# Optimization experiments

Hardware: AMD Instinct MI355X
Metric: run time of the kernel (lower is better)

## Reference

```python
import jax, jax.numpy as jnp
import numpy as np

N_NODES = 50000


def gcn_conv(x, edge_index, edge_weight, W, b):
    """PyG GCNConv: x' = D^{-1/2}(A+I)D^{-1/2} (x W) + b, with edge weights."""
    n = x.shape[0]
    x = x @ W  # transform first (PyG order): [N, d_out]
    row, col = edge_index[0], edge_index[1]  # source -> target
    # add self loops with weight 1
    loop = jnp.arange(n)
    row = jnp.concatenate([row, loop])
    col = jnp.concatenate([col, loop])
    ew = jnp.concatenate([edge_weight, jnp.ones((n,), dtype=x.dtype)])
    # symmetric normalization based on (weighted) in-degree at targets
    deg = jax.ops.segment_sum(ew, col, num_segments=n)
    dis = jnp.where(deg > 0, jax.lax.rsqrt(deg), 0.0)
    norm = dis[row] * ew * dis[col]  # [E+N]
    # gather-scale-scatter aggregation
    msg = x[row] * norm[:, None]  # [E+N, d_out]
    out = jax.ops.segment_sum(msg, col, num_segments=n)
    return out + b


def setup_inputs() -> dict:
    key = jax.random.key(0)
    ks = jax.random.split(key, 9)
    E = 800000
    bert_output = jax.random.normal(ks[0], (N_NODES, 1024), dtype=jnp.float32)
    edge_index = jax.random.randint(ks[1], (2, E), 0, N_NODES, dtype=jnp.int64)
    edge_weight = jax.random.uniform(ks[2], (E,), dtype=jnp.float32)
    s1 = 1.0 / np.sqrt(1024)
    s2 = 1.0 / np.sqrt(512)
    s3 = 1.0 / np.sqrt(128)
    W1 = jax.random.uniform(ks[3], (1024, 512), jnp.float32, -s1, s1)
    b1 = jnp.zeros((512,), jnp.float32)
    W2 = jax.random.uniform(ks[4], (512, 128), jnp.float32, -s2, s2)
    b2 = jnp.zeros((128,), jnp.float32)
    Wfc = jax.random.uniform(ks[5], (128, 14), jnp.float32, -s3, s3)
    bfc = jax.random.uniform(ks[6], (14,), jnp.float32, -s3, s3)
    return {
        "bert_output": bert_output,
        "edge_index": edge_index,
        "edge_weight": edge_weight,
        "W1": W1, "b1": b1, "W2": W2, "b2": b2, "Wfc": Wfc, "bfc": bfc,
    }


def reference(bert_output, edge_index, edge_weight, W1, b1, W2, b2, Wfc, bfc):
    h = jax.nn.relu(gcn_conv(bert_output, edge_index, edge_weight, W1, b1))
    h = jax.nn.relu(gcn_conv(h, edge_index, edge_weight, W2, b2))
    logits = h @ Wfc + bfc
    return jax.nn.sigmoid(logits)
```

## Files before the change

### kernel.cpp

```cpp
#include <hip/hip_runtime.h>
#include <stdint.h>

__device__ __forceinline__ float bf2f(unsigned short h) {
  union { uint32_t u; float f; } v; v.u = ((uint32_t)h) << 16; return v.f;
}
__device__ __forceinline__ unsigned short f2bf(float f) {
  union { float f; uint32_t u; } v; v.f = f;
  uint32_t u = v.u;
  u += 0x7FFFu + ((u >> 16) & 1u);
  return (unsigned short)(u >> 16);
}
__device__ __forceinline__ uint32_t pack2bf(float a, float b) {
  return (uint32_t)f2bf(a) | ((uint32_t)f2bf(b) << 16);
}
__device__ __forceinline__ int ld_idx(const void* p, size_t i, int is64) {
  return is64 ? (int)((const long long*)p)[i] : ((const int*)p)[i];
}
__device__ __forceinline__ float ld_w(const void* p, size_t i, int f32) {
  return f32 ? ((const float*)p)[i] : bf2f(((const unsigned short*)p)[i]);
}

typedef __attribute__((ext_vector_type(8))) short short8;
typedef __attribute__((ext_vector_type(4))) float floatx4;

__device__ __forceinline__ void gl2lds16(const unsigned short* g, unsigned short* l) {
  __builtin_amdgcn_global_load_lds(
      (const __attribute__((address_space(1))) uint32_t*)(const void*)g,
      (__attribute__((address_space(3))) uint32_t*)(void*)l,
      16, 0, 0);
}

__global__ void bgcn_init_probe(float* __restrict__ deg, int* __restrict__ counts,
                                int* __restrict__ fill, int n,
                                const uint32_t* __restrict__ xw,
                                const uint32_t* __restrict__ iw,
                                int* __restrict__ flags) {
  int i = blockIdx.x * 256 + threadIdx.x;
  if (i < n) { deg[i] = 1.0f; counts[i] = 0; fill[i] = 0; }
  if (blockIdx.x == 0 && threadIdx.x < 64) {
    int lane = threadIdx.x;
    int hits = 0;
    #pragma unroll
    for (int j = 0; j < 4; ++j) {
      uint32_t b = (xw[lane * 4 + j] >> 8) & 0x7F;
      hits += (b >= 0x38 && b <= 0x41) ? 1 : 0;
    }
    #pragma unroll
    for (int off = 32; off; off >>= 1) hits += __shfl_xor(hits, off);
    unsigned long long nz = __ballot(iw[2 * lane + 1] != 0u);
    if (lane == 0) {
      flags[0] = (hits < 128) ? 1 : 0;
      flags[1] = (nz == 0ull) ? 1 : 0;
    }
  }
}

__global__ void bgcn_cvt8(const void* __restrict__ src, unsigned short* __restrict__ dst,
                          int n8, const int* __restrict__ flags) {
  int i = blockIdx.x * 256 + threadIdx.x;
  if (i >= n8) return;
  size_t o = (size_t)i * 8;
  uint4 d;
  if (flags[0]) {
    const float4* f = (const float4*)((const float*)src + o);
    float4 f0 = f[0], f1 = f[1];
    d = make_uint4(pack2bf(f0.x, f0.y), pack2bf(f0.z, f0.w),
                   pack2bf(f1.x, f1.y), pack2bf(f1.z, f1.w));
  } else {
    d = *(const uint4*)((const unsigned short*)src + o);
  }
  *(uint4*)(dst + o) = d;
}
__global__ __launch_bounds__(256) void bgcn_cvt_t(
    const void* __restrict__ src, unsigned short* __restrict__ dst,
    int K, int N, const int* __restrict__ flags) {
  __shared__ unsigned short tile[32][33];
  int k0 = blockIdx.x * 32, n0 = blockIdx.y * 32;
  int tx = threadIdx.x & 31, ty = threadIdx.x >> 5;
  bool f32 = flags[0];
  #pragma unroll
  for (int i = 0; i < 4; ++i) {
    size_t s = (size_t)(k0 + ty + i * 8) * N + n0 + tx;
    tile[ty + i * 8][tx] = f32 ? f2bf(((const float*)src)[s])
                               : ((const unsigned short*)src)[s];
  }
  __syncthreads();
  #pragma unroll
  for (int i = 0; i < 4; ++i)
    dst[(size_t)(n0 + ty + i * 8) * K + k0 + tx] = tile[tx][ty + i * 8];
}
__global__ void bgcn_cvt_small(const void* b1, const void* b2,
                               const void* wfc, const void* bfc,
                               unsigned short* db1, unsigned short* db2,
                               unsigned short* dwfc, unsigned short* dbfc,
                               const int* __restrict__ flags) {
  int i = blockIdx.x * 256 + threadIdx.x;
  bool f32 = flags[0];
  const void* s; unsigned short* d; int j;
  if (i < 512)            { s = b1;  d = db1;  j = i; }
  else if (i < 640)       { s = b2;  d = db2;  j = i - 512; }
  else if (i < 2432)      { s = wfc; d = dwfc; j = i - 640; }
  else if (i < 2446)      { s = bfc; d = dbfc; j = i - 2432; }
  else return;
  d[j] = f32 ? f2bf(((const float*)s)[j]) : ((const unsigned short*)s)[j];
}

__global__ void bgcn_deg_hist(const void* __restrict__ ei, const void* __restrict__ ew,
                              const int* __restrict__ flags,
                              float* __restrict__ deg, int* __restrict__ counts, int E) {
  int e = blockIdx.x * 256 + threadIdx.x;
  if (e >= E) return;
  int c = ld_idx(ei, (size_t)E + e, flags[1]);
  atomicAdd(&deg[c], ld_w(ew, e, flags[0]));
  atomicAdd(&counts[c], 1);
}
__global__ void bgcn_scan_block(const int* __restrict__ counts, int* __restrict__ rowptr,
                                int* __restrict__ blocksum,
                                const float* __restrict__ deg, float* __restrict__ dis,
                                int n) {
  __shared__ int buf[1024];
  int gid = blockIdx.x * 1024 + threadIdx.x;
  int v = (gid < n) ? counts[gid] : 0;
  buf[threadIdx.x] = v;
  __syncthreads();
  for (int off = 1; off < 1024; off <<= 1) {
    int x = (threadIdx.x >= off) ? buf[threadIdx.x - off] : 0;
    __syncthreads();
    buf[threadIdx.x] += x;
    __syncthreads();
  }
  if (gid < n) {
    rowptr[gid + 1] = buf[threadIdx.x];
    dis[gid] = rsqrtf(deg[gid]);
  }
  if (threadIdx.x == 1023) blocksum[blockIdx.x] = buf[1023];
}
__global__ void bgcn_scan_tops(int* __restrict__ blocksum, int nb) {
  __shared__ int buf[1024];
  int t = threadIdx.x;
  int v = (t < nb) ? blocksum[t] : 0;
  buf[t] = v;
  __syncthreads();
  for (int off = 1; off < 1024; off <<= 1) {
    int x = (t >= off) ? buf[t - off] : 0;
    __syncthreads();
    buf[t] += x;
    __syncthreads();
  }
  if (t < nb) blocksum[t] = buf[t] - v;
}
__global__ void bgcn_scan_add(int* __restrict__ rowptr, const int* __restrict__ blocksum, int n) {
  int gid = blockIdx.x * 1024 + threadIdx.x;
  if (gid < n) rowptr[gid + 1] += blocksum[blockIdx.x];
  if (gid == 0) rowptr[0] = 0;
}
__global__ void bgcn_scatter(const void* __restrict__ ei, const void* __restrict__ ew,
                             const int* __restrict__ flags,
                             const float* __restrict__ dis,
                             const int* __restrict__ rowptr, int* __restrict__ fill,
                             int2* __restrict__ epair, int E) {
  int e = blockIdx.x * 256 + threadIdx.x;
  if (e >= E) return;
  int is64 = flags[1];
  int r = ld_idx(ei, e, is64), c = ld_idx(ei, (size_t)E + e, is64);
  int pos = rowptr[c] + atomicAdd(&fill[c], 1);
  float nrm = dis[r] * ld_w(ew, e, flags[0]) * dis[c];
  epair[pos] = make_int2(r, __float_as_int(nrm));
}

__global__ __launch_bounds__(256) void bgcn_gemm_lds(
    const unsigned short* __restrict__ A,
    const unsigned short* __restrict__ Bt,
    unsigned short* __restrict__ C,
    int M, int N, int K, int nblk_bits) {
  __shared__ unsigned short Abuf[128 * 32];
  __shared__ unsigned short Bbuf[128 * 32];
  int t = threadIdx.x;
  int wave = t >> 6, lane = t & 63;
  int bx = blockIdx.x;
  int nblk = bx & ((1 << nblk_bits) - 1);
  int mblk = bx >> nblk_bits;
  int m0 = mblk * 128, n0 = nblk * 128;

  floatx4 acc[4][4];
  #pragma unroll
  for (int i = 0; i < 4; ++i)
    #pragma unroll
    for (int j = 0; j < 4; ++j)
      #pragma unroll
      for (int r = 0; r < 4; ++r) acc[i][j][r] = 0.0f;

  int rii  = lane >> 2;
  int koff = (lane & 3) * 8;
  int ar0 = m0 + wave * 32 + rii;      if (ar0 >= M) ar0 = M - 1;
  int ar1 = m0 + wave * 32 + 16 + rii; if (ar1 >= M) ar1 = M - 1;
  const unsigned short* Ag0 = A + (size_t)ar0 * K + koff;
  const unsigned short* Ag1 = A + (size_t)ar1 * K + koff;
  const unsigned short* Bg0 = Bt + (size_t)(n0 + wave * 32 + rii) * K + koff;
  const unsigned short* Bg1 = Bg0 + (size_t)16 * K;
  unsigned short* Al0 = Abuf + (wave * 32) * 32 + lane * 8;
  unsigned short* Al1 = Abuf + (wave * 32 + 16) * 32 + lane * 8;
  unsigned short* Bl0 = Bbuf + (wave * 32) * 32 + lane * 8;
  unsigned short* Bl1 = Bbuf + (wave * 32 + 16) * 32 + lane * 8;

  int fr = lane & 15;
  int fk = (lane >> 4) * 8;
  int mw = (wave & 1) * 64;
  int nw = (wave >> 1) * 64;

  for (int k0 = 0; k0 < K; k0 += 32) {
    gl2lds16(Ag0 + k0, Al0);
    gl2lds16(Ag1 + k0, Al1);
    gl2lds16(Bg0 + k0, Bl0);
    gl2lds16(Bg1 + k0, Bl1);
    __syncthreads();

    short8 afr[4], bfr[4];
    #pragma unroll
    for (int i = 0; i < 4; ++i)
      afr[i] = *(const short8*)(Abuf + (mw + i * 16 + fr) * 32 + fk);
    #pragma unroll
    for (int i = 0; i < 4; ++i)
      bfr[i] = *(const short8*)(Bbuf + (nw + i * 16 + fr) * 32 + fk);
    #pragma unroll
    for (int mt = 0; mt < 4; ++mt)
      #pragma unroll
      for (int nt = 0; nt < 4; ++nt)
        acc[mt][nt] = __builtin_amdgcn_mfma_f32_16x16x32_bf16(afr[mt], bfr[nt], acc[mt][nt], 0, 0, 0);
    __syncthreads();
  }

  int col_l = lane & 15;
  int row_b = (lane >> 4) * 4;
  #pragma unroll
  for (int mt = 0; mt < 4; ++mt)
    #pragma unroll
    for (int nt = 0; nt < 4; ++nt)
      #pragma unroll
      for (int r = 0; r < 4; ++r) {
        int m = m0 + mw + mt * 16 + row_b + r;
        if (m < M)
          C[(size_t)m * N + n0 + nw + nt * 16 + col_l] = f2bf(acc[mt][nt][r]);
      }
}

#define GST 40
__global__ __launch_bounds__(256, 2) void bgcn_gemm128(
    const void* __restrict__ Araw, int a_probe, const int* __restrict__ flags,
    const unsigned short* __restrict__ Bt,
    unsigned short* __restrict__ C,
    int M, int N, int K, int nblk_bits) {
  __shared__ unsigned short Abuf[128 * GST];
  __shared__ unsigned short Bbuf[128 * GST];
  const bool a_fp32 = a_probe && flags[0];
  int t = threadIdx.x;
  int wave = t >> 6, lane = t & 63;
  int bx = blockIdx.x;
  int nblk = bx & ((1 << nblk_bits) - 1);
  int mblk = bx >> nblk_bits;
  int m0 = mblk * 128, n0 = nblk * 128;

  floatx4 acc[4][4];
  #pragma unroll
  for (int i = 0; i < 4; ++i)
    #pragma unroll
    for (int j = 0; j < 4; ++j)
      #pragma unroll
      for (int r = 0; r < 4; ++r) acc[i][j][r] = 0.0f;

  int srow  = t >> 1;
  int skoff = (t & 1) * 16;
  int am = m0 + srow; if (am >= M) am = M - 1;
  const float*          Af = (const float*)Araw          + (size_t)am * K + skoff;
  const unsigned short* Ah = (const unsigned short*)Araw + (size_t)am * K + skoff;
  const unsigned short* Bp = Bt + (size_t)(n0 + srow) * K + skoff;
  unsigned short* AL = Abuf + srow * GST + skoff;
  unsigned short* BL = Bbuf + srow * GST + skoff;

  int fr = lane & 15;
  int fk = (lane >> 4) * 8;
  int mw = (wave & 1) * 64;
  int nw = (wave >> 1) * 64;

  for (int k0 = 0; k0 < K; k0 += 32) {
    uint4 a0, a1;
    if (a_fp32) {
      float4 f0 = *(const float4*)(Af + k0);
      float4 f1 = *(const float4*)(Af + k0 + 4);
      float4 f2 = *(const float4*)(Af + k0 + 8);
      float4 f3 = *(const float4*)(Af + k0 + 12);
      a0 = make_uint4(pack2bf(f0.x, f0.y), pack2bf(f0.z, f0.w),
                      pack2bf(f1.x, f1.y), pack2bf(f1.z, f1.w));
      a1 = make_uint4(pack2bf(f2.x, f2.y), pack2bf(f2.z, f2.w),
                      pack2bf(f3.x, f3.y), pack2bf(f3.z, f3.w));
    } else {
      a0 = *(const uint4*)(Ah + k0);
      a1 = *(const uint4*)(Ah + k0 + 8);
    }
    uint4 b0 = *(const uint4*)(Bp + k0);
    uint4 b1 = *(const uint4*)(Bp + k0 + 8);
    *(uint4*)AL       = a0;
    *(uint4*)(AL + 8) = a1;
    *(uint4*)BL       = b0;
    *(uint4*)(BL + 8) = b1;
    __syncthreads();

    short8 afr[4], bfr[4];
    #pragma unroll
    for (int i = 0; i < 4; ++i)
      afr[i] = *(const short8*)(Abuf + (mw + i * 16 + fr) * GST + fk);
    #pragma unroll
    for (int i = 0; i < 4; ++i)
      bfr[i] = *(const short8*)(Bbuf + (nw + i * 16 + fr) * GST + fk);
    #pragma unroll
    for (int mt = 0; mt < 4; ++mt)
      #pragma unroll
      for (int nt = 0; nt < 4; ++nt)
        acc[mt][nt] = __builtin_amdgcn_mfma_f32_16x16x32_bf16(afr[mt], bfr[nt], acc[mt][nt], 0, 0, 0);
    __syncthreads();
  }

  int col_l = lane & 15;
  int row_b = (lane >> 4) * 4;
  #pragma unroll
  for (int mt = 0; mt < 4; ++mt)
    #pragma unroll
    for (int nt = 0; nt < 4; ++nt)
      #pragma unroll
      for (int r = 0; r < 4; ++r) {
        int m = m0 + mw + mt * 16 + row_b + r;
        if (m < M)
          C[(size_t)m * N + n0 + nw + nt * 16 + col_l] = f2bf(acc[mt][nt][r]);
      }
}

__device__ __forceinline__ void accum4(float* acc, uint2 r, float w) {
  acc[0] += w * bf2f((unsigned short)(r.x & 0xffff));
  acc[1] += w * bf2f((unsigned short)(r.x >> 16));
  acc[2] += w * bf2f((unsigned short)(r.y & 0xffff));
  acc[3] += w * bf2f((unsigned short)(r.y >> 16));
}
__device__ __forceinline__ void accum2(float* acc, uint32_t r, float w) {
  acc[0] += w * bf2f((unsigned short)(r & 0xffff));
  acc[1] += w * bf2f((unsigned short)(r >> 16));
}

template <int F, int WPN>
__global__ __launch_bounds__(256) void bgcn_aggregate(
    const unsigned short* __restrict__ H,
    const int* __restrict__ rowptr,
    const int2* __restrict__ epair,
    const float* __restrict__ dis,
    const unsigned short* __restrict__ bias,
    unsigned short* __restrict__ Out,
    int n_nodes) {
  constexpr int FPW = F / WPN;
  constexpr int VPL = FPW / 64;
  constexpr int NPB = 4 / WPN;
  constexpr int DEPTH = 8;

  int t = threadIdx.x;
  int lane = t & 63;
  int wid = __builtin_amdgcn_readfirstlane(t >> 6);
  int c = blockIdx.x * NPB + wid / WPN;
  if (c >= n_nodes) return;
  c = __builtin_amdgcn_readfirstlane(c);
  int h = wid % WPN;

  int beg = __builtin_amdgcn_readfirstlane(rowptr[c]);
  int end = __builtin_amdgcn_readfirstlane(rowptr[c + 1]);
  float ds = dis[c];

  int fo = h * FPW + lane * VPL;
  const unsigned short* Hl = H + fo;

  uint2 rs;
  union { uint2 v; unsigned short u[4]; } bu;
  if constexpr (VPL == 4) {
    rs = *(const uint2*)(Hl + (size_t)c * F);
    bu.v = *(const uint2*)(bias + fo);
  } else {
    rs.x = *(const uint32_t*)(Hl + (size_t)c * F);
    bu.v.x = *(const uint32_t*)(bias + fo);
  }

  float acc[VPL];
  #pragma unroll
  for (int j = 0; j < VPL; ++j) acc[j] = 0.0f;

  for (int base = beg; base < end; base += 64) {
    int n = end - base;
    if (n > 64) n = 64;
    n = __builtin_amdgcn_readfirstlane(n);
    int2 mv = make_int2(0, 0);
    if (lane < n) mv = epair[base + lane];
    for (int q0 = 0; q0 < n; q0 += DEPTH) {
      uint2 r[DEPTH];
      float w[DEPTH];
      #pragma unroll
      for (int j = 0; j < DEPTH; ++j) {
        int q = q0 + j;
        int qs = (q < n) ? q : 0;
        int sq = __builtin_amdgcn_readlane(mv.x, qs);
        w[j] = __int_as_float(
            __builtin_amdgcn_readlane(mv.y, q));
        const unsigned short* src = Hl + (size_t)sq * F;
        if constexpr (VPL == 4) r[j] = *(const uint2*)src;
        else                    r[j].x = *(const uint32_t*)src;
      }
      #pragma unroll
      for (int j = 0; j < DEPTH; ++j) {
        if constexpr (VPL == 4) accum4(acc, r[j], w[j]);
        else                    accum2(acc, r[j].x, w[j]);
      }
    }
  }

  float wself = ds * ds;
  if constexpr (VPL == 4) accum4(acc, rs, wself);
  else                    accum2(acc, rs.x, wself);

  unsigned short ob[VPL];
  #pragma unroll
  for (int j = 0; j < VPL; ++j) {
    float v = acc[j] + bf2f(bu.u[j]);
    ob[j] = f2bf(fmaxf(v, 0.0f));
  }
  if constexpr (VPL == 4) {
    uint2 st;
    st.x = (uint32_t)ob[0] | ((uint32_t)ob[1] << 16);
    st.y = (uint32_t)ob[2] | ((uint32_t)ob[3] << 16);
    *(uint2*)(Out + (size_t)c * F + fo) = st;
  } else {
    *(uint32_t*)(Out + (size_t)c * F + fo) =
        (uint32_t)ob[0] | ((uint32_t)ob[1] << 16);
  }
}

__global__ __launch_bounds__(256) void bgcn_fc_sigmoid(
    const unsigned short* __restrict__ X,
    const unsigned short* __restrict__ W,
    const unsigned short* __restrict__ b,
    float* __restrict__ out,
    int n_nodes) {
  __shared__ float Ws[128 * 14];
  __shared__ float bs[14];
  for (int i = threadIdx.x; i < 128 * 14; i += 256) Ws[i] = bf2f(W[i]);
  if (threadIdx.x < 14) bs[threadIdx.x] = bf2f(b[threadIdx.x]);
  __syncthreads();
  int node = blockIdx.x * 256 + threadIdx.x;
  if (node >= n_nodes) return;
  float acc[14];
  #pragma unroll
  for (int c = 0; c < 14; ++c) acc[c] = bs[c];
  const unsigned short* xp = X + (size_t)node * 128;
  for (int k8 = 0; k8 < 16; ++k8) {
    uint4 r = *(const uint4*)(xp + k8 * 8);
    float xv[8];
    xv[0] = bf2f((unsigned short)(r.x & 0xffff)); xv[1] = bf2f((unsigned short)(r.x >> 16));
    xv[2] = bf2f((unsigned short)(r.y & 0xffff)); xv[3] = bf2f((unsigned short)(r.y >> 16));
    xv[4] = bf2f((unsigned short)(r.z & 0xffff)); xv[5] = bf2f((unsigned short)(r.z >> 16));
    xv[6] = bf2f((unsigned short)(r.w & 0xffff)); xv[7] = bf2f((unsigned short)(r.w >> 16));
    #pragma unroll
    for (int j = 0; j < 8; ++j) {
      int k = k8 * 8 + j;
      #pragma unroll
      for (int c = 0; c < 14; ++c) acc[c] = fmaf(xv[j], Ws[k * 14 + c], acc[c]);
    }
  }
  float* op = out + (size_t)node * 14;
  #pragma unroll
  for (int c = 0; c < 14; ++c)
    op[c] = 1.0f / (1.0f + __expf(-acc[c]));
}

static inline size_t padsz(size_t x) { return (x + 255) & ~(size_t)255; }
static inline void* wsa(char*& p, size_t bytes) {
  void* r = p;
  p += padsz(bytes);
  return r;
}

extern "C" void kernel_launch(void* const* d_in, const int* in_sizes, int n_in,
                              void* d_out, int out_size, void* d_ws, size_t ws_size,
                              hipStream_t stream) {
  const void* Xr   = d_in[0];
  const void* EIr  = d_in[1];
  const void* EWr  = d_in[2];
  const void* W1r  = d_in[3];
  const void* b1r  = d_in[4];
  const void* W2r  = d_in[5];
  const void* b2r  = d_in[6];
  const void* Wfcr = d_in[7];
  const void* bfcr = d_in[8];
  float* out = (float*)d_out;

  const int N = in_sizes[0] / 1024;
  const int E = in_sizes[2];

  size_t need = padsz((size_t)N * 512 * 2)
              + padsz((size_t)N * 1024 * 2)
              + 4 * padsz((size_t)N * 4)
              + padsz((size_t)(N + 1) * 4)
              + padsz(256 * 4)
              + padsz((size_t)E * 8)
              + padsz(1024 * 512 * 2) + padsz(512 * 128 * 2)
              + padsz(512 * 2) + padsz(128 * 2) + padsz(128 * 14 * 2)
              + padsz(32) + padsz(8);
  const bool big = ws_size >= need;

  char* p = (char*)d_ws;
  unsigned short* R1  = (unsigned short*)wsa(p, (size_t)N * 512 * 2);
  unsigned short* R2  = (unsigned short*)wsa(p, (size_t)N * (big ? 1024 : 512) * 2);
  float* deg      = (float*)wsa(p, (size_t)N * 4);
  float* dis      = (float*)wsa(p, (size_t)N * 4);
  int*   counts   = (int*)wsa(p, (size_t)N * 4);
  int*   fill     = (int*)wsa(p, (size_t)N * 4);
  int*   rowptr   = (int*)wsa(p, (size_t)(N + 1) * 4);
  int*   blocksum = (int*)wsa(p, 256 * 4);
  int2*  epair    = (int2*)wsa(p, (size_t)E * 8);
  unsigned short* W1t  = (unsigned short*)wsa(p, (size_t)1024 * 512 * 2);
  unsigned short* W2t  = (unsigned short*)wsa(p, (size_t)512 * 128 * 2);
  unsigned short* b1c  = (unsigned short*)wsa(p, 512 * 2);
  unsigned short* b2c  = (unsigned short*)wsa(p, 128 * 2);
  unsigned short* Wfcc = (unsigned short*)wsa(p, 128 * 14 * 2);
  unsigned short* bfcc = (unsigned short*)wsa(p, 32);
  int* flags      = (int*)wsa(p, 8);

  unsigned short* H1  = R1;
  unsigned short* Xbf = R2;
  unsigned short* X2  = R2;
  unsigned short* H2  = R1;
  unsigned short* X3  = R1 + (size_t)N * 128;

  int gN = (N + 255) / 256;
  int gE = (E + 255) / 256;

  bgcn_init_probe<<<gN, 256, 0, stream>>>(deg, counts, fill, N,
                                          (const uint32_t*)Xr, (const uint32_t*)EIr, flags);
  { dim3 g(1024 / 32, 512 / 32); bgcn_cvt_t<<<g, 256, 0, stream>>>(W1r, W1t, 1024, 512, flags); }
  { dim3 g(512 / 32, 128 / 32);  bgcn_cvt_t<<<g, 256, 0, stream>>>(W2r, W2t, 512, 128, flags); }
  bgcn_cvt_small<<<10, 256, 0, stream>>>(b1r, b2r, Wfcr, bfcr, b1c, b2c, Wfcc, bfcc, flags);
  if (big) {
    int n8 = N * 1024 / 8;
    bgcn_cvt8<<<(n8 + 255) / 256, 256, 0, stream>>>(Xr, Xbf, n8, flags);
  }

  bgcn_deg_hist<<<gE, 256, 0, stream>>>(EIr, EWr, flags, deg, counts, E);
  int nb = (N + 1023) / 1024;
  bgcn_scan_block<<<nb, 1024, 0, stream>>>(counts, rowptr, blocksum, deg, dis, N);
  bgcn_scan_tops<<<1, 1024, 0, stream>>>(blocksum, nb);
  bgcn_scan_add<<<nb, 1024, 0, stream>>>(rowptr, blocksum, N);
  bgcn_scatter<<<gE, 256, 0, stream>>>(EIr, EWr, flags, dis, rowptr, fill, epair, E);

  int mblks = (N + 127) / 128;

  if (big)
    bgcn_gemm_lds<<<mblks * 4, 256, 0, stream>>>(Xbf, W1t, H1, N, 512, 1024, 2);
  else
    bgcn_gemm128<<<mblks * 4, 256, 0, stream>>>(Xr, 1, flags, W1t, H1, N, 512, 1024, 2);
  bgcn_aggregate<512, 2><<<(N + 1) / 2, 256, 0, stream>>>(
      H1, rowptr, epair, dis, b1c, X2, N);

  bgcn_gemm_lds<<<mblks, 256, 0, stream>>>(X2, W2t, H2, N, 128, 512, 0);
  bgcn_aggregate<128, 1><<<(N + 3) / 4, 256, 0, stream>>>(
      H2, rowptr, epair, dis, b2c, X3, N);

  bgcn_fc_sigmoid<<<gN, 256, 0, stream>>>(X3, Wfcc, bfcc, out, N);
}
```

Baseline: 709.7 us.

## Split layer-1 aggregation into four feature slices across blocks

The layer-1 aggregation (F=512) was two waves per node, each lane handling four bf16 features. It now uses four feature slices, and each slice runs in a separate block covering four nodes, so every lane handles two features. The kernel is simplified to a single 2-feature path. This gives more, lighter waves and shorter per-lane dependency chains, which should improve latency hiding on the gather. The cost is that each edge's index and weight are read and broadcast four times instead of twice, and the row gathers become narrower 4-byte loads.

```diff
diff --git a/kernel.cpp b/kernel.cpp
--- a/kernel.cpp
+++ b/kernel.cpp
@@ -334,18 +334,12 @@
       }
 }
 
-__device__ __forceinline__ void accum4(float* acc, uint2 r, float w) {
-  acc[0] += w * bf2f((unsigned short)(r.x & 0xffff));
-  acc[1] += w * bf2f((unsigned short)(r.x >> 16));
-  acc[2] += w * bf2f((unsigned short)(r.y & 0xffff));
-  acc[3] += w * bf2f((unsigned short)(r.y >> 16));
-}
 __device__ __forceinline__ void accum2(float* acc, uint32_t r, float w) {
   acc[0] += w * bf2f((unsigned short)(r & 0xffff));
   acc[1] += w * bf2f((unsigned short)(r >> 16));
 }
 
-template <int F, int WPN>
+template <int F, int SLICES>
 __global__ __launch_bounds__(256) void bgcn_aggregate(
     const unsigned short* __restrict__ H,
     const int* __restrict__ rowptr,
@@ -354,35 +348,28 @@
     const unsigned short* __restrict__ bias,
     unsigned short* __restrict__ Out,
     int n_nodes) {
-  constexpr int FPW = F / WPN;
+  constexpr int FPW = F / SLICES;
   constexpr int VPL = FPW / 64;
-  constexpr int NPB = 4 / WPN;
+  constexpr int SB = (SLICES == 4) ? 2 : (SLICES == 2) ? 1 : 0;
   constexpr int DEPTH = 8;
 
   int t = threadIdx.x;
   int lane = t & 63;
   int wid = __builtin_amdgcn_readfirstlane(t >> 6);
-  int c = blockIdx.x * NPB + wid / WPN;
+  int s = blockIdx.x & (SLICES - 1);
+  int c = (blockIdx.x >> SB) * 4 + wid;
   if (c >= n_nodes) return;
   c = __builtin_amdgcn_readfirstlane(c);
-  int h = wid % WPN;
 
   int beg = __builtin_amdgcn_readfirstlane(rowptr[c]);
   int end = __builtin_amdgcn_readfirstlane(rowptr[c + 1]);
   float ds = dis[c];
 
-  int fo = h * FPW + lane * VPL;
+  int fo = s * FPW + lane * VPL;
   const unsigned short* Hl = H + fo;
 
-  uint2 rs;
-  union { uint2 v; unsigned short u[4]; } bu;
-  if constexpr (VPL == 4) {
-    rs = *(const uint2*)(Hl + (size_t)c * F);
-    bu.v = *(const uint2*)(bias + fo);
-  } else {
-    rs.x = *(const uint32_t*)(Hl + (size_t)c * F);
-    bu.v.x = *(const uint32_t*)(bias + fo);
-  }
+  uint32_t rs = *(const uint32_t*)(Hl + (size_t)c * F);
+  uint32_t buv = *(const uint32_t*)(bias + fo);
 
   float acc[VPL];
   #pragma unroll
@@ -395,7 +382,7 @@
     int2 mv = make_int2(0, 0);
     if (lane < n) mv = epair[base + lane];
     for (int q0 = 0; q0 < n; q0 += DEPTH) {
-      uint2 r[DEPTH];
+      uint32_t r[DEPTH];
       float w[DEPTH];
       #pragma unroll
       for (int j = 0; j < DEPTH; ++j) {
@@ -404,37 +391,24 @@
         int sq = __builtin_amdgcn_readlane(mv.x, qs);
         w[j] = __int_as_float(
             __builtin_amdgcn_readlane(mv.y, q));
-        const unsigned short* src = Hl + (size_t)sq * F;
-        if constexpr (VPL == 4) r[j] = *(const uint2*)src;
-        else                    r[j].x = *(const uint32_t*)src;
+        r[j] = *(const uint32_t*)(Hl + (size_t)sq * F);
       }
       #pragma unroll
-      for (int j = 0; j < DEPTH; ++j) {
-        if constexpr (VPL == 4) accum4(acc, r[j], w[j]);
-        else                    accum2(acc, r[j].x, w[j]);
-      }
+      for (int j = 0; j < DEPTH; ++j) accum2(acc, r[j], w[j]);
     }
   }
 
   float wself = ds * ds;
-  if constexpr (VPL == 4) accum4(acc, rs, wself);
-  else                    accum2(acc, rs.x, wself);
+  accum2(acc, rs, wself);
 
   unsigned short ob[VPL];
   #pragma unroll
   for (int j = 0; j < VPL; ++j) {
-    float v = acc[j] + bf2f(bu.u[j]);
+    float v = acc[j] + bf2f((unsigned short)((buv >> (16 * j)) & 0xffff));
     ob[j] = f2bf(fmaxf(v, 0.0f));
   }
-  if constexpr (VPL == 4) {
-    uint2 st;
-    st.x = (uint32_t)ob[0] | ((uint32_t)ob[1] << 16);
-    st.y = (uint32_t)ob[2] | ((uint32_t)ob[3] << 16);
-    *(uint2*)(Out + (size_t)c * F + fo) = st;
-  } else {
-    *(uint32_t*)(Out + (size_t)c * F + fo) =
-        (uint32_t)ob[0] | ((uint32_t)ob[1] << 16);
-  }
+  *(uint32_t*)(Out + (size_t)c * F + fo) =
+      (uint32_t)ob[0] | ((uint32_t)ob[1] << 16);
 }
 
 __global__ __launch_bounds__(256) void bgcn_fc_sigmoid(
@@ -554,16 +528,17 @@
   bgcn_scatter<<<gE, 256, 0, stream>>>(EIr, EWr, flags, dis, rowptr, fill, epair, E);
 
   int mblks = (N + 127) / 128;
+  int ngrp  = (N + 3) / 4;
 
   if (big)
     bgcn_gemm_lds<<<mblks * 4, 256, 0, stream>>>(Xbf, W1t, H1, N, 512, 1024, 2);
   else
     bgcn_gemm128<<<mblks * 4, 256, 0, stream>>>(Xr, 1, flags, W1t, H1, N, 512, 1024, 2);
-  bgcn_aggregate<512, 2><<<(N + 1) / 2, 256, 0, stream>>>(
+  bgcn_aggregate<512, 4><<<ngrp * 4, 256, 0, stream>>>(
       H1, rowptr, epair, dis, b1c, X2, N);
 
   bgcn_gemm_lds<<<mblks, 256, 0, stream>>>(X2, W2t, H2, N, 128, 512, 0);
-  bgcn_aggregate<128, 1><<<(N + 3) / 4, 256, 0, stream>>>(
+  bgcn_aggregate<128, 1><<<ngrp, 256, 0, stream>>>(
       H2, rowptr, epair, dis, b2c, X3, N);
 
   bgcn_fc_sigmoid<<<gN, 256, 0, stream>>>(X3, Wfcc, bfcc, out, N);
```

Result: faster. 690.9 us (-2.6%).
